# Performance work log

Measured on AMD Instinct MI355X. Metric: run time of the kernel, lower is better.

## Reference

```python
import jax, jax.numpy as jnp
import numpy as np

CUTOFF = 1.6  # short_range_cutoff from init_kwargs
E = 20_000_000
N_ATOMS = 100_000


def setup_inputs() -> dict:
    key = jax.random.key(0)
    k1, k2, k3 = jax.random.split(key, 3)
    Rij = jax.random.normal(k1, (E, 3), dtype=jnp.float32)
    idx_i = jax.random.randint(k2, (E,), 0, N_ATOMS, dtype=jnp.int32)
    idx_j = jax.random.randint(k3, (E,), 0, N_ATOMS, dtype=jnp.int32)
    return {"Rij": Rij, "idx_i": idx_i, "idx_j": idx_j}


def reference(Rij, idx_i, idx_j):
    """Faithful jit-compatible version of FilterShortRange.forward.

    torch.nonzero produces a dynamic-size index list; under jit we use the
    static-size equivalent jnp.nonzero(size=E, fill_value=0) and a validity
    mask: the first n_sr entries of the compacted outputs are exactly the
    short-range edges (same order as torch), padding beyond n_sr is zeroed
    (indices set to -1).
    """
    rij = jnp.linalg.norm(Rij, axis=-1)              # [E] per-edge distance
    mask = rij <= CUTOFF                             # [E] bool
    n_sr = jnp.sum(mask)                             # number of short-range edges
    (cidx,) = jnp.nonzero(mask, size=E, fill_value=0)  # stable compaction indices
    valid = jnpp_arange(E) < n_sr if False else (jnp.arange(E) < n_sr)  # [E]
    Rij_sr = jnp.where(valid[:, None], Rij[cidx], 0.0)   # [E,3], first n_sr rows valid
    idx_i_sr = jnp.where(valid, idx_i[cidx], -1)
    idx_j_sr = jnp.where(valid, idx_j[cidx], -1)
    # (Rij_lr, idx_i_lr, idx_j_lr, Rij, idx_i, idx_j, count)
    return (Rij, idx_i, idx_j, Rij_sr, idx_i_sr, idx_j_sr, n_sr)
```

## Files before the change

### kernel.cpp

```cpp
#include <hip/hip_runtime.h>

#define CUTOFF 1.6f
#define BLOCK 256
#define EPT 8
#define EPB (BLOCK * EPT)

struct f3 { float x, y, z; };

__global__ void __launch_bounds__(BLOCK) k1_count_copy(
    const float* __restrict__ Rij, float* __restrict__ outRij,
    int* __restrict__ counts, long E)
{
  long b = blockIdx.x;
  int t = threadIdx.x;
  long base = b * (long)EPB + (long)t * EPT;
  int cnt = 0;
  if (base < E) {
    const f3* rp = (const f3*)Rij;
    f3* op = (f3*)outRij;
#pragma unroll
    for (int k = 0; k < EPT; ++k) {
      f3 v = rp[base + k];
      op[base + k] = v;
      float s = sqrtf(v.x * v.x + v.y * v.y + v.z * v.z);
      cnt += (s <= CUTOFF) ? 1 : 0;
    }
  }
#pragma unroll
  for (int d = 32; d > 0; d >>= 1) cnt += __shfl_down(cnt, d, 64);
  __shared__ int ssum;
  if (t == 0) ssum = 0;
  __syncthreads();
  if ((t & 63) == 0) atomicAdd(&ssum, cnt);
  __syncthreads();
  if (t == 0) counts[b] = ssum;
}

__global__ void __launch_bounds__(1024) k2_scan(
    int* __restrict__ counts, int nb, int* __restrict__ nsr,
    float* __restrict__ out_nsr)
{
  int t = threadIdx.x;
  int C = (nb + 1023) >> 10;
  int start = t * C;
  int end = min(start + C, nb);
  int sum = 0;
  for (int i = start; i < end; ++i) sum += counts[i];
  int lane = t & 63, wid = t >> 6;
  int v = sum;
#pragma unroll
  for (int d = 1; d < 64; d <<= 1) {
    int n = __shfl_up(v, d, 64);
    if (lane >= d) v += n;
  }
  __shared__ int wsum[16];
  if (lane == 63) wsum[wid] = v;
  __syncthreads();
  int woff = 0;
  for (int w = 0; w < wid; ++w) woff += wsum[w];
  int run = woff + v - sum;
  for (int i = start; i < end; ++i) {
    int c = counts[i];
    counts[i] = run;
    run += c;
  }
  if (t == 1023) {
    nsr[0] = run;
    out_nsr[0] = (float)run;
  }
}

__global__ void __launch_bounds__(256) k4_fill(
    float* __restrict__ out, const int* __restrict__ nsr, long E)
{
  long n = *nsr;
  long stride = (long)gridDim.x * blockDim.x;
  f3* sr = (f3*)(out + 5 * E);
  float* oi = out + 8 * E;
  float* oj = out + 9 * E;
  for (long i = n + (long)blockIdx.x * blockDim.x + threadIdx.x; i < E;
       i += stride) {
    f3 z{0.f, 0.f, 0.f};
    sr[i] = z;
    oi[i] = -1.0f;
    oj[i] = -1.0f;
  }
}

__global__ void __launch_bounds__(BLOCK) k3_scatter(
    const float* __restrict__ Rij, const int* __restrict__ idx_i,
    const int* __restrict__ idx_j, const int* __restrict__ offs,
    float* __restrict__ out, long E)
{
  long b = blockIdx.x;
  int t = threadIdx.x;
  long base = b * (long)EPB + (long)t * EPT;
  f3 v[EPT];
  int ii[EPT], jj[EPT];
  unsigned m = 0;
  int cnt = 0;
  if (base < E) {
    const f3* rp = (const f3*)Rij;
#pragma unroll
    for (int k = 0; k < EPT; ++k) v[k] = rp[base + k];
    const int4* ip = (const int4*)(idx_i + base);
    const int4* jp = (const int4*)(idx_j + base);
    int4 ia = ip[0], ib = ip[1], ja = jp[0], jb = jp[1];
    ii[0] = ia.x; ii[1] = ia.y; ii[2] = ia.z; ii[3] = ia.w;
    ii[4] = ib.x; ii[5] = ib.y; ii[6] = ib.z; ii[7] = ib.w;
    jj[0] = ja.x; jj[1] = ja.y; jj[2] = ja.z; jj[3] = ja.w;
    jj[4] = jb.x; jj[5] = jb.y; jj[6] = jb.z; jj[7] = jb.w;
    float4 fi0 = make_float4((float)ii[0], (float)ii[1], (float)ii[2], (float)ii[3]);
    float4 fi1 = make_float4((float)ii[4], (float)ii[5], (float)ii[6], (float)ii[7]);
    float4 fj0 = make_float4((float)jj[0], (float)jj[1], (float)jj[2], (float)jj[3]);
    float4 fj1 = make_float4((float)jj[4], (float)jj[5], (float)jj[6], (float)jj[7]);
    *(float4*)(out + 3 * E + base) = fi0;
    *(float4*)(out + 3 * E + base + 4) = fi1;
    *(float4*)(out + 4 * E + base) = fj0;
    *(float4*)(out + 4 * E + base + 4) = fj1;
#pragma unroll
    for (int k = 0; k < EPT; ++k) {
      float s = sqrtf(v[k].x * v[k].x + v[k].y * v[k].y + v[k].z * v[k].z);
      if (s <= CUTOFF) { m |= 1u << k; ++cnt; }
    }
  }
  int lane = t & 63, wid = t >> 6;
  int sv = cnt;
#pragma unroll
  for (int d = 1; d < 64; d <<= 1) {
    int n = __shfl_up(sv, d, 64);
    if (lane >= d) sv += n;
  }
  __shared__ int wsum[BLOCK / 64];
  if (lane == 63) wsum[wid] = sv;
  __syncthreads();
  int woff = 0;
#pragma unroll
  for (int w = 0; w < BLOCK / 64; ++w)
    if (w < wid) woff += wsum[w];
  long pos = (long)offs[b] + woff + (sv - cnt);
  if (base < E && m) {
    f3* srp = (f3*)(out + 5 * E);
    float* oi = out + 8 * E;
    float* oj = out + 9 * E;
#pragma unroll
    for (int k = 0; k < EPT; ++k) {
      if (m & (1u << k)) {
        srp[pos] = v[k];
        oi[pos] = (float)ii[k];
        oj[pos] = (float)jj[k];
        ++pos;
      }
    }
  }
}

extern "C" void kernel_launch(void* const* d_in, const int* in_sizes, int n_in,
                              void* d_out, int out_size, void* d_ws,
                              size_t ws_size, hipStream_t stream)
{
  const float* Rij = (const float*)d_in[0];
  const int* idx_i = (const int*)d_in[1];
  const int* idx_j = (const int*)d_in[2];
  long E = (long)in_sizes[1];
  float* out = (float*)d_out;

  int nb = (int)((E + EPB - 1) / EPB);
  int* counts = (int*)d_ws;
  int* nsr = counts + nb;

  k1_count_copy<<<nb, BLOCK, 0, stream>>>(Rij, out, counts, E);
  k2_scan<<<1, 1024, 0, stream>>>(counts, nb, nsr, out + 10 * E);
  k4_fill<<<2048, 256, 0, stream>>>(out, nsr, E);
  k3_scatter<<<nb, BLOCK, 0, stream>>>(Rij, idx_i, idx_j, counts, out, E);
}
```

Measured before the change: 341.0 us.

## Fuse count, scan and scatter into single-pass decoupled look-back kernel

Replaces the three-kernel count/scan/scatter pipeline with one kernel that computes block counts, publishes aggregate and inclusive prefix flags in a workspace array, and uses wavefront-parallel decoupled look-back to get each block's offset. Rij is now read once instead of twice, and it is loaded as float4 vectors. A memset of the flag array is added, and correctness relies on blocks being scheduled roughly in order and on relaxed atomics being visible across blocks. Block ordering is taken from blockIdx, which assumes forward-progress dispatch order.

```diff
diff --git a/kernel.cpp b/kernel.cpp
--- a/kernel.cpp
+++ b/kernel.cpp
@@ -5,72 +5,152 @@
 #define EPT 8
 #define EPB (BLOCK * EPT)
 
+#define ST_INV 0ull
+#define ST_AGG (1ull << 62)
+#define ST_PRE (2ull << 62)
+
 struct f3 { float x, y, z; };
 
-__global__ void __launch_bounds__(BLOCK) k1_count_copy(
-    const float* __restrict__ Rij, float* __restrict__ outRij,
-    int* __restrict__ counts, long E)
+__global__ void __launch_bounds__(BLOCK) k_main(
+    const float* __restrict__ Rij, const int* __restrict__ idx_i,
+    const int* __restrict__ idx_j, float* __restrict__ out,
+    unsigned long long* __restrict__ ts, int* __restrict__ nsr,
+    long E, int nb)
 {
   long b = blockIdx.x;
   int t = threadIdx.x;
+  int lane = t & 63, wid = t >> 6;
   long base = b * (long)EPB + (long)t * EPT;
+
+  float rr[24];
+  int ii[EPT], jj[EPT];
+  unsigned m = 0;
   int cnt = 0;
+
   if (base < E) {
-    const f3* rp = (const f3*)Rij;
-    f3* op = (f3*)outRij;
+    const float4* rp4 = (const float4*)(Rij + base * 3);
+    float4* op4 = (float4*)(out + base * 3);
+#pragma unroll
+    for (int q = 0; q < 6; ++q) {
+      float4 v = rp4[q];
+      op4[q] = v;
+      rr[q * 4 + 0] = v.x; rr[q * 4 + 1] = v.y;
+      rr[q * 4 + 2] = v.z; rr[q * 4 + 3] = v.w;
+    }
+    const int4* ip = (const int4*)(idx_i + base);
+    const int4* jp = (const int4*)(idx_j + base);
+    int4 ia = ip[0], ib = ip[1], ja = jp[0], jb = jp[1];
+    ii[0] = ia.x; ii[1] = ia.y; ii[2] = ia.z; ii[3] = ia.w;
+    ii[4] = ib.x; ii[5] = ib.y; ii[6] = ib.z; ii[7] = ib.w;
+    jj[0] = ja.x; jj[1] = ja.y; jj[2] = ja.z; jj[3] = ja.w;
+    jj[4] = jb.x; jj[5] = jb.y; jj[6] = jb.z; jj[7] = jb.w;
 #pragma unroll
     for (int k = 0; k < EPT; ++k) {
-      f3 v = rp[base + k];
-      op[base + k] = v;
-      float s = sqrtf(v.x * v.x + v.y * v.y + v.z * v.z);
-      cnt += (s <= CUTOFF) ? 1 : 0;
+      float x = rr[3 * k], y = rr[3 * k + 1], z = rr[3 * k + 2];
+      float s = sqrtf(x * x + y * y + z * z);
+      if (s <= CUTOFF) { m |= 1u << k; ++cnt; }
     }
   }
-#pragma unroll
-  for (int d = 32; d > 0; d >>= 1) cnt += __shfl_down(cnt, d, 64);
-  __shared__ int ssum;
-  if (t == 0) ssum = 0;
-  __syncthreads();
-  if ((t & 63) == 0) atomicAdd(&ssum, cnt);
-  __syncthreads();
-  if (t == 0) counts[b] = ssum;
-}
 
-__global__ void __launch_bounds__(1024) k2_scan(
-    int* __restrict__ counts, int nb, int* __restrict__ nsr,
-    float* __restrict__ out_nsr)
-{
-  int t = threadIdx.x;
-  int C = (nb + 1023) >> 10;
-  int start = t * C;
-  int end = min(start + C, nb);
-  int sum = 0;
-  for (int i = start; i < end; ++i) sum += counts[i];
-  int lane = t & 63, wid = t >> 6;
-  int v = sum;
+  int sv = cnt;
 #pragma unroll
   for (int d = 1; d < 64; d <<= 1) {
-    int n = __shfl_up(v, d, 64);
-    if (lane >= d) v += n;
+    int n = __shfl_up(sv, d, 64);
+    if (lane >= d) sv += n;
   }
-  __shared__ int wsum[16];
-  if (lane == 63) wsum[wid] = v;
+  __shared__ int wsum[BLOCK / 64];
+  __shared__ int sh_excl;
+  if (lane == 63) wsum[wid] = sv;
   __syncthreads();
-  int woff = 0;
-  for (int w = 0; w < wid; ++w) woff += wsum[w];
-  int run = woff + v - sum;
-  for (int i = start; i < end; ++i) {
-    int c = counts[i];
-    counts[i] = run;
-    run += c;
+  int woff = 0, bsum = 0;
+#pragma unroll
+  for (int w = 0; w < BLOCK / 64; ++w) {
+    int s = wsum[w];
+    if (w < wid) woff += s;
+    bsum += s;
   }
-  if (t == 1023) {
-    nsr[0] = run;
-    out_nsr[0] = (float)run;
+  int texcl = woff + sv - cnt;
+
+  if (wid == 0) {
+    if (lane == 0 && b > 0) {
+      __hip_atomic_store(&ts[b], (unsigned long long)bsum | ST_AGG,
+                         __ATOMIC_RELAXED, __HIP_MEMORY_SCOPE_AGENT);
+    }
+    long excl = 0;
+    if (b > 0) {
+      int pred = (int)b - 1;
+      for (;;) {
+        int i = pred - lane;
+        unsigned long long s =
+            (i >= 0) ? __hip_atomic_load(&ts[i], __ATOMIC_RELAXED,
+                                         __HIP_MEMORY_SCOPE_AGENT)
+                     : 0ull;
+        unsigned st = (unsigned)(s >> 62);
+        int val = (int)(s & 0xFFFFFFFFull);
+        unsigned long long invm = __ballot(st == 0u);
+        unsigned long long prfm = __ballot(st == 2u);
+        int mm = invm ? (__ffsll((long long)invm) - 1) : 64;
+        int pp = prfm ? (__ffsll((long long)prfm) - 1) : 64;
+        if (pp < mm) {
+          int c = (lane <= pp) ? val : 0;
+#pragma unroll
+          for (int d = 32; d; d >>= 1) c += __shfl_down(c, d, 64);
+          excl += c;
+          break;
+        } else if (mm > 0) {
+          int c = (lane < mm) ? val : 0;
+#pragma unroll
+          for (int d = 32; d; d >>= 1) c += __shfl_down(c, d, 64);
+          excl += c;
+          pred -= mm;
+        } else {
+          __builtin_amdgcn_s_sleep(1);
+        }
+      }
+    }
+    if (lane == 0) {
+      long inc = excl + bsum;
+      __hip_atomic_store(&ts[b], (unsigned long long)inc | ST_PRE,
+                         __ATOMIC_RELAXED, __HIP_MEMORY_SCOPE_AGENT);
+      sh_excl = (int)excl;
+      if (b == (long)nb - 1) {
+        nsr[0] = (int)inc;
+        out[10 * E] = (float)inc;
+      }
+    }
+  }
+
+  if (base < E) {
+    float4 fi0 = make_float4((float)ii[0], (float)ii[1], (float)ii[2], (float)ii[3]);
+    float4 fi1 = make_float4((float)ii[4], (float)ii[5], (float)ii[6], (float)ii[7]);
+    float4 fj0 = make_float4((float)jj[0], (float)jj[1], (float)jj[2], (float)jj[3]);
+    float4 fj1 = make_float4((float)jj[4], (float)jj[5], (float)jj[6], (float)jj[7]);
+    *(float4*)(out + 3 * E + base) = fi0;
+    *(float4*)(out + 3 * E + base + 4) = fi1;
+    *(float4*)(out + 4 * E + base) = fj0;
+    *(float4*)(out + 4 * E + base + 4) = fj1;
+  }
+  __syncthreads();
+
+  long pos = (long)sh_excl + texcl;
+  if (base < E && m) {
+    f3* srp = (f3*)(out + 5 * E);
+    float* oi = out + 8 * E;
+    float* oj = out + 9 * E;
+#pragma unroll
+    for (int k = 0; k < EPT; ++k) {
+      if (m & (1u << k)) {
+        f3 v{rr[3 * k], rr[3 * k + 1], rr[3 * k + 2]};
+        srp[pos] = v;
+        oi[pos] = (float)ii[k];
+        oj[pos] = (float)jj[k];
+        ++pos;
+      }
+    }
   }
 }
 
-__global__ void __launch_bounds__(256) k4_fill(
+__global__ void __launch_bounds__(256) k_fill(
     float* __restrict__ out, const int* __restrict__ nsr, long E)
 {
   long n = *nsr;
@@ -87,74 +167,6 @@
   }
 }
 
-__global__ void __launch_bounds__(BLOCK) k3_scatter(
-    const float* __restrict__ Rij, const int* __restrict__ idx_i,
-    const int* __restrict__ idx_j, const int* __restrict__ offs,
-    float* __restrict__ out, long E)
-{
-  long b = blockIdx.x;
-  int t = threadIdx.x;
-  long base = b * (long)EPB + (long)t * EPT;
-  f3 v[EPT];
-  int ii[EPT], jj[EPT];
-  unsigned m = 0;
-  int cnt = 0;
-  if (base < E) {
-    const f3* rp = (const f3*)Rij;
-#pragma unroll
-    for (int k = 0; k < EPT; ++k) v[k] = rp[base + k];
-    const int4* ip = (const int4*)(idx_i + base);
-    const int4* jp = (const int4*)(idx_j + base);
-    int4 ia = ip[0], ib = ip[1], ja = jp[0], jb = jp[1];
-    ii[0] = ia.x; ii[1] = ia.y; ii[2] = ia.z; ii[3] = ia.w;
-    ii[4] = ib.x; ii[5] = ib.y; ii[6] = ib.z; ii[7] = ib.w;
-    jj[0] = ja.x; jj[1] = ja.y; jj[2] = ja.z; jj[3] = ja.w;
-    jj[4] = jb.x; jj[5] = jb.y; jj[6] = jb.z; jj[7] = jb.w;
-    float4 fi0 = make_float4((float)ii[0], (float)ii[1], (float)ii[2], (float)ii[3]);
-    float4 fi1 = make_float4((float)ii[4], (float)ii[5], (float)ii[6], (float)ii[7]);
-    float4 fj0 = make_float4((float)jj[0], (float)jj[1], (float)jj[2], (float)jj[3]);
-    float4 fj1 = make_float4((float)jj[4], (float)jj[5], (float)jj[6], (float)jj[7]);
-    *(float4*)(out + 3 * E + base) = fi0;
-    *(float4*)(out + 3 * E + base + 4) = fi1;
-    *(float4*)(out + 4 * E + base) = fj0;
-    *(float4*)(out + 4 * E + base + 4) = fj1;
-#pragma unroll
-    for (int k = 0; k < EPT; ++k) {
-      float s = sqrtf(v[k].x * v[k].x + v[k].y * v[k].y + v[k].z * v[k].z);
-      if (s <= CUTOFF) { m |= 1u << k; ++cnt; }
-    }
-  }
-  int lane = t & 63, wid = t >> 6;
-  int sv = cnt;
-#pragma unroll
-  for (int d = 1; d < 64; d <<= 1) {
-    int n = __shfl_up(sv, d, 64);
-    if (lane >= d) sv += n;
-  }
-  __shared__ int wsum[BLOCK / 64];
-  if (lane == 63) wsum[wid] = sv;
-  __syncthreads();
-  int woff = 0;
-#pragma unroll
-  for (int w = 0; w < BLOCK / 64; ++w)
-    if (w < wid) woff += wsum[w];
-  long pos = (long)offs[b] + woff + (sv - cnt);
-  if (base < E && m) {
-    f3* srp = (f3*)(out + 5 * E);
-    float* oi = out + 8 * E;
-    float* oj = out + 9 * E;
-#pragma unroll
-    for (int k = 0; k < EPT; ++k) {
-      if (m & (1u << k)) {
-        srp[pos] = v[k];
-        oi[pos] = (float)ii[k];
-        oj[pos] = (float)jj[k];
-        ++pos;
-      }
-    }
-  }
-}
-
 extern "C" void kernel_launch(void* const* d_in, const int* in_sizes, int n_in,
                               void* d_out, int out_size, void* d_ws,
                               size_t ws_size, hipStream_t stream)
@@ -166,11 +178,11 @@
   float* out = (float*)d_out;
 
   int nb = (int)((E + EPB - 1) / EPB);
-  int* counts = (int*)d_ws;
-  int* nsr = counts + nb;
+  unsigned long long* ts = (unsigned long long*)d_ws;
+  int* nsr = (int*)(ts + nb);
 
-  k1_count_copy<<<nb, BLOCK, 0, stream>>>(Rij, out, counts, E);
-  k2_scan<<<1, 1024, 0, stream>>>(counts, nb, nsr, out + 10 * E);
-  k4_fill<<<2048, 256, 0, stream>>>(out, nsr, E);
-  k3_scatter<<<nb, BLOCK, 0, stream>>>(Rij, idx_i, idx_j, counts, out, E);
+  hipMemsetAsync(d_ws, 0, (size_t)nb * 8, stream);
+
+  k_main<<<nb, BLOCK, 0, stream>>>(Rij, idx_i, idx_j, out, ts, nsr, E, nb);
+  k_fill<<<2048, 256, 0, stream>>>(out, nsr, E);
 }
```

After: 441.0 us. +29.4%, slower.
